# Kernel optimization log

Measured on AMD Instinct MI355X. Metric: run time of the kernel, lower is better.

## Reference

```python
import jax, jax.numpy as jnp
import numpy as np

B, S, D = 2, 2048, 2048
H = 16
HD = D // H
SCALE = 1.0 / (HD ** 0.5)


def setup_inputs() -> dict:
    key = jax.random.key(0)
    ks = jax.random.split(key, 9)
    std = 0.02
    return {
        "x": jax.random.normal(ks[0], (B, S, D), dtype=jnp.float32),
        "q_w": jax.random.normal(ks[1], (D, D), dtype=jnp.float32) * std,
        "q_b": jax.random.normal(ks[2], (D,), dtype=jnp.float32) * std,
        "k_w": jax.random.normal(ks[3], (D, D), dtype=jnp.float32) * std,
        "k_b": jax.random.normal(ks[4], (D,), dtype=jnp.float32) * std,
        "v_w": jax.random.normal(ks[5], (D, D), dtype=jnp.float32) * std,
        "v_b": jax.random.normal(ks[6], (D,), dtype=jnp.float32) * std,
        "o_w": jax.random.normal(ks[7], (D, D), dtype=jnp.float32) * std,
        "o_b": jax.random.normal(ks[8], (D,), dtype=jnp.float32) * std,
    }


def reference(x, q_w, q_b, k_w, k_b, v_w, v_b, o_w, o_b):
    # torch Linear: y = x @ W.T + b  (weights stored [out, in])
    b, s, _ = x.shape
    dtype = x.dtype
    q = (x @ q_w.T + q_b).reshape(b, s, H, HD).transpose(0, 2, 1, 3)  # [B,H,S,HD]
    k = (x @ k_w.T + k_b).reshape(b, s, H, HD).transpose(0, 2, 1, 3)
    v = (x @ v_w.T + v_b).reshape(b, s, H, HD).transpose(0, 2, 1, 3)
    scores = jnp.einsum("bhqd,bhkd->bhqk", q, k) * SCALE  # [B,H,S,S]
    # causal mask: positions k > q get -inf (via triu(diagonal=1))
    causal = jnp.triu(jnp.ones((s, s), dtype=bool), k=1)
    scores = jnp.where(causal[None, None], -jnp.inf, scores)
    attn = jax.nn.softmax(scores.astype(jnp.float32), axis=-1).astype(dtype)
    out = jnp.einsum("bhqk,bhkd->bhqd", attn, v)  # [B,H,S,HD]
    out = out.transpose(0, 2, 1, 3).reshape(b, s, H * HD)
    return out @ o_w.T + o_b
```

## Files before the change

kernel.cpp:

```cpp
#include <hip/hip_runtime.h>
#include <hip/hip_bf16.h>

#define S_LEN 2048
#define DMODEL 2048
#define NH 16
#define HDIM 128
#define SCALE_F 0.08838834764831845f

typedef __attribute__((ext_vector_type(8))) short bf16x8;
typedef __attribute__((ext_vector_type(4))) float f32x4;

__device__ __forceinline__ unsigned short f2bf(float f) {
  unsigned int u = __float_as_uint(f);
  u += 0x7FFFu + ((u >> 16) & 1u);
  return (unsigned short)(u >> 16);
}

__device__ __forceinline__ void gload16(const void* g, void* l) {
  __builtin_amdgcn_global_load_lds(
      (const __attribute__((address_space(1))) unsigned int*)g,
      (__attribute__((address_space(3))) unsigned int*)l, 16, 0, 0);
}

__global__ __launch_bounds__(256) void cvt_f32_bf16(
    const float* __restrict__ in, unsigned short* __restrict__ out, int n4) {
  int i = blockIdx.x * blockDim.x + threadIdx.x;
  if (i < n4) {
    const float4 v = *(const float4*)(in + i * 4);
    ushort4 o;
    o.x = f2bf(v.x); o.y = f2bf(v.y); o.z = f2bf(v.z); o.w = f2bf(v.w);
    *(ushort4*)(out + i * 4) = o;
  }
}

__global__ __launch_bounds__(256, 2) void gemm_qkv(
    const unsigned short* __restrict__ A,
    const unsigned short* __restrict__ W,
    const float* __restrict__ qbias, const float* __restrict__ kbias,
    const float* __restrict__ vbias,
    unsigned short* __restrict__ qo, unsigned short* __restrict__ ko,
    unsigned short* __restrict__ vto) {
  __shared__ unsigned short As[128 * 32];
  __shared__ unsigned short Bs[128 * 32];
  const int t = threadIdx.x;
  const int lane = t & 63;
  const int w = t >> 6;
  const int m0 = blockIdx.x * 128;
  const int n0 = blockIdx.y * 128;
  const int wr = w >> 1, wc = w & 1;

  f32x4 acc[4][4];
#pragma unroll
  for (int i = 0; i < 4; i++)
#pragma unroll
    for (int j = 0; j < 4; j++)
#pragma unroll
      for (int e = 0; e < 4; e++) acc[i][j][e] = 0.f;

  const int r0 = t >> 2;
  const int kc0 = (t & 3) * 8;
  const unsigned short* Arow0 = A + (m0 + r0) * DMODEL + kc0;
  const unsigned short* Arow1 = A + (m0 + 64 + r0) * DMODEL + kc0;
  const unsigned short* Wrow0 = W + (n0 + r0) * DMODEL + kc0;
  const unsigned short* Wrow1 = W + (n0 + 64 + r0) * DMODEL + kc0;
  char* AsB = (char*)As;
  char* BsB = (char*)Bs;

  const int frow = lane & 15;
  const int fcol = (lane >> 4) * 8;

  for (int k0 = 0; k0 < DMODEL; k0 += 32) {
    __syncthreads();
    gload16(Arow0 + k0, AsB + w * 1024);
    gload16(Arow1 + k0, AsB + 4096 + w * 1024);
    gload16(Wrow0 + k0, BsB + w * 1024);
    gload16(Wrow1 + k0, BsB + 4096 + w * 1024);
    __syncthreads();
    bf16x8 af[4], bfr[4];
#pragma unroll
    for (int i = 0; i < 4; i++)
      af[i] = *(const bf16x8*)&As[(wr * 64 + i * 16 + frow) * 32 + fcol];
#pragma unroll
    for (int j = 0; j < 4; j++)
      bfr[j] = *(const bf16x8*)&Bs[(wc * 64 + j * 16 + frow) * 32 + fcol];
#pragma unroll
    for (int i = 0; i < 4; i++)
#pragma unroll
      for (int j = 0; j < 4; j++)
        acc[i][j] = __builtin_amdgcn_mfma_f32_16x16x32_bf16(af[i], bfr[j],
                                                            acc[i][j], 0, 0, 0);
  }

  const int b_ = m0 >> 11;
  const int proj = n0 >> 11;
  const int nn_base = (n0 & 2047) + wc * 64;
  const float* bias = (proj == 0) ? qbias : ((proj == 1) ? kbias : vbias);
#pragma unroll
  for (int j = 0; j < 4; j++) {
    const int nn = nn_base + j * 16 + (lane & 15);
    const int h = nn >> 7, hd = nn & 127;
    const float bv = bias[nn];
#pragma unroll
    for (int i = 0; i < 4; i++) {
      const int mrow = m0 + wr * 64 + i * 16 + (lane >> 4) * 4;
      const int s = mrow & 2047;
      if (proj == 2) {
        unsigned short* dst = vto + ((b_ * NH + h) * HDIM + hd) * S_LEN + s;
        ushort4 pk;
        pk.x = f2bf(acc[i][j][0] + bv);
        pk.y = f2bf(acc[i][j][1] + bv);
        pk.z = f2bf(acc[i][j][2] + bv);
        pk.w = f2bf(acc[i][j][3] + bv);
        *(ushort4*)dst = pk;
      } else {
        unsigned short* dst =
            ((proj == 0) ? qo : ko) + ((b_ * NH + h) * S_LEN + s) * HDIM + hd;
#pragma unroll
        for (int r = 0; r < 4; r++) dst[r * HDIM] = f2bf(acc[i][j][r] + bv);
      }
    }
  }
}

__global__ __launch_bounds__(256, 2) void attn_fwd(
    const unsigned short* __restrict__ Q,
    const unsigned short* __restrict__ K,
    const unsigned short* __restrict__ VT,
    unsigned short* __restrict__ ctx) {
  __shared__ unsigned short Ks[2][64 * 128];
  __shared__ unsigned short Vs[2][128 * 64];
  __shared__ unsigned short Ps[4][16 * 64];
  const int t = threadIdx.x, lane = t & 63, w = t >> 6;
  const int bh = blockIdx.y;
  const unsigned short* Qb = Q + bh * (S_LEN * HDIM);
  const unsigned short* Kb = K + bh * (S_LEN * HDIM);
  const unsigned short* Vb = VT + bh * (HDIM * S_LEN);
  const int b_ = bh >> 4, h = bh & 15;

  const int krow_s = t >> 2;
  const int kchunk = t & 3;

  auto stageKV = [&](int buf, int kv0) {
#pragma unroll
    for (int u = 0; u < 4; ++u) {
      const int c = t + u * 256;
      const int row = c >> 4, cc = c & 15;
      gload16(Kb + (kv0 + row) * HDIM + ((cc ^ (row & 7)) * 8),
              (char*)Ks[buf] + u * 4096 + w * 1024);
    }
#pragma unroll
    for (int u = 0; u < 4; ++u) {
      const int c = t + u * 256;
      const int row = c >> 3, cc = c & 7;
      gload16(Vb + row * S_LEN + kv0 + ((cc ^ (row & 7)) * 8),
              (char*)Vs[buf] + u * 4096 + w * 1024);
    }
  };

#pragma unroll 1
  for (int pi = 0; pi < 2; ++pi) {
    const int qtile = pi ? (31 - blockIdx.x) : blockIdx.x;
    const int q0 = qtile * 64 + w * 16;

    bf16x8 qf[4];
    {
      const unsigned short* qrow =
          Qb + (q0 + (lane & 15)) * HDIM + (lane >> 4) * 8;
#pragma unroll
      for (int dk = 0; dk < 4; dk++) qf[dk] = *(const bf16x8*)(qrow + dk * 32);
    }

    float mrow[4], lrow[4];
    f32x4 oacc[8];
#pragma unroll
    for (int r = 0; r < 4; r++) { mrow[r] = -__builtin_inff(); lrow[r] = 0.f; }
#pragma unroll
    for (int d = 0; d < 8; d++)
#pragma unroll
      for (int e = 0; e < 4; e++) oacc[d][e] = 0.f;

    const int nt = qtile + 1;
    stageKV(0, 0);
    __syncthreads();
    int cur = 0;

#pragma unroll 1
    for (int kt = 0; kt < nt; ++kt) {
      if (kt + 1 < nt) stageKV(cur ^ 1, (kt + 1) * 64);

      const unsigned short* Kc = Ks[cur];
      const unsigned short* Vc = Vs[cur];
      const int kv0 = kt * 64;

      f32x4 sacc[4];
#pragma unroll
      for (int ck = 0; ck < 4; ck++)
#pragma unroll
        for (int e = 0; e < 4; e++) sacc[ck][e] = 0.f;
      __builtin_amdgcn_s_setprio(1);
#pragma unroll
      for (int ck = 0; ck < 4; ++ck) {
        const int krow = ck * 16 + (lane & 15);
#pragma unroll
        for (int dk = 0; dk < 4; ++dk) {
          const int chunk = dk * 4 + (lane >> 4);
          const bf16x8 kf = *(const bf16x8*)((const char*)Kc + krow * 256 +
                                             ((chunk ^ (krow & 7)) << 4));
          sacc[ck] = __builtin_amdgcn_mfma_f32_16x16x32_bf16(qf[dk], kf,
                                                             sacc[ck], 0, 0, 0);
        }
      }
      __builtin_amdgcn_s_setprio(0);
#pragma unroll
      for (int ck = 0; ck < 4; ck++)
#pragma unroll
        for (int r = 0; r < 4; r++) sacc[ck][r] *= SCALE_F;
      if (kt == qtile) {
#pragma unroll
        for (int ck = 0; ck < 4; ck++) {
          const int col = kv0 + ck * 16 + (lane & 15);
#pragma unroll
          for (int r = 0; r < 4; r++) {
            const int rowq = q0 + (lane >> 4) * 4 + r;
            if (col > rowq) sacc[ck][r] = -__builtin_inff();
          }
        }
      }
      float tmax[4];
#pragma unroll
      for (int r = 0; r < 4; r++)
        tmax[r] = fmaxf(fmaxf(sacc[0][r], sacc[1][r]),
                        fmaxf(sacc[2][r], sacc[3][r]));
#pragma unroll
      for (int off = 1; off < 16; off <<= 1)
#pragma unroll
        for (int r = 0; r < 4; r++)
          tmax[r] = fmaxf(tmax[r], __shfl_xor(tmax[r], off, 64));
      bool need = false;
#pragma unroll
      for (int r = 0; r < 4; r++) need |= (tmax[r] > mrow[r] + 8.f);
      if (__any(need)) {
#pragma unroll
        for (int r = 0; r < 4; r++) {
          const float mn = fmaxf(mrow[r], tmax[r]);
          const float corr = __expf(mrow[r] - mn);
          mrow[r] = mn;
          lrow[r] *= corr;
#pragma unroll
          for (int d = 0; d < 8; d++) oacc[d][r] *= corr;
        }
      }
      float rsum[4] = {0.f, 0.f, 0.f, 0.f};
#pragma unroll
      for (int ck = 0; ck < 4; ck++)
#pragma unroll
        for (int r = 0; r < 4; r++) {
          const float p = __expf(sacc[ck][r] - mrow[r]);
          rsum[r] += p;
          const int prow = (lane >> 4) * 4 + r;
          const int pcol = ck * 16 + (lane & 15);
          *(unsigned short*)((char*)Ps[w] +
                             ((prow * 128 + pcol * 2) ^ ((prow & 7) << 4))) =
              f2bf(p);
        }
#pragma unroll
      for (int off = 1; off < 16; off <<= 1)
#pragma unroll
        for (int r = 0; r < 4; r++) rsum[r] += __shfl_xor(rsum[r], off, 64);
#pragma unroll
      for (int r = 0; r < 4; r++) lrow[r] += rsum[r];

      bf16x8 pf[2];
      {
        const int prow = lane & 15;
#pragma unroll
        for (int kk = 0; kk < 2; kk++) {
          const int chunk = kk * 4 + (lane >> 4);
          pf[kk] = *(const bf16x8*)((const char*)Ps[w] + prow * 128 +
                                    ((chunk ^ (prow & 7)) << 4));
        }
      }
      __builtin_amdgcn_s_setprio(1);
#pragma unroll
      for (int d = 0; d < 8; ++d) {
        const int vrow = d * 16 + (lane & 15);
#pragma unroll
        for (int kk = 0; kk < 2; ++kk) {
          const int chunk = kk * 4 + (lane >> 4);
          const bf16x8 vf = *(const bf16x8*)((const char*)Vc + vrow * 128 +
                                             ((chunk ^ (vrow & 7)) << 4));
          oacc[d] = __builtin_amdgcn_mfma_f32_16x16x32_bf16(pf[kk], vf, oacc[d],
                                                            0, 0, 0);
        }
      }
      __builtin_amdgcn_s_setprio(0);

      __syncthreads();
      cur ^= 1;
    }

#pragma unroll
    for (int r = 0; r < 4; r++) {
      const float inv = 1.f / lrow[r];
      const int srow = q0 + (lane >> 4) * 4 + r;
      unsigned short* dst =
          ctx + (b_ * S_LEN + srow) * DMODEL + h * HDIM + (lane & 15);
#pragma unroll
      for (int d = 0; d < 8; d++) dst[d * 16] = f2bf(oacc[d][r] * inv);
    }
  }
}

__global__ __launch_bounds__(256, 2) void gemm_out(
    const unsigned short* __restrict__ A,
    const unsigned short* __restrict__ W,
    const float* __restrict__ bias, float* __restrict__ out) {
  __shared__ unsigned short As[128 * 32];
  __shared__ unsigned short Bs[128 * 32];
  const int t = threadIdx.x;
  const int lane = t & 63;
  const int w = t >> 6;
  const int m0 = blockIdx.x * 128;
  const int n0 = blockIdx.y * 128;
  const int wr = w >> 1, wc = w & 1;

  f32x4 acc[4][4];
#pragma unroll
  for (int i = 0; i < 4; i++)
#pragma unroll
    for (int j = 0; j < 4; j++)
#pragma unroll
      for (int e = 0; e < 4; e++) acc[i][j][e] = 0.f;

  const int r0 = t >> 2;
  const int kc0 = (t & 3) * 8;
  const unsigned short* Arow0 = A + (m0 + r0) * DMODEL + kc0;
  const unsigned short* Arow1 = A + (m0 + 64 + r0) * DMODEL + kc0;
  const unsigned short* Wrow0 = W + (n0 + r0) * DMODEL + kc0;
  const unsigned short* Wrow1 = W + (n0 + 64 + r0) * DMODEL + kc0;
  char* AsB = (char*)As;
  char* BsB = (char*)Bs;
  const int frow = lane & 15;
  const int fcol = (lane >> 4) * 8;

  for (int k0 = 0; k0 < DMODEL; k0 += 32) {
    __syncthreads();
    gload16(Arow0 + k0, AsB + w * 1024);
    gload16(Arow1 + k0, AsB + 4096 + w * 1024);
    gload16(Wrow0 + k0, BsB + w * 1024);
    gload16(Wrow1 + k0, BsB + 4096 + w * 1024);
    __syncthreads();
    bf16x8 af[4], bfr[4];
#pragma unroll
    for (int i = 0; i < 4; i++)
      af[i] = *(const bf16x8*)&As[(wr * 64 + i * 16 + frow) * 32 + fcol];
#pragma unroll
    for (int j = 0; j < 4; j++)
      bfr[j] = *(const bf16x8*)&Bs[(wc * 64 + j * 16 + frow) * 32 + fcol];
#pragma unroll
    for (int i = 0; i < 4; i++)
#pragma unroll
      for (int j = 0; j < 4; j++)
        acc[i][j] = __builtin_amdgcn_mfma_f32_16x16x32_bf16(af[i], bfr[j],
                                                            acc[i][j], 0, 0, 0);
  }

#pragma unroll
  for (int j = 0; j < 4; j++) {
    const int n = n0 + wc * 64 + j * 16 + (lane & 15);
    const float bv = bias[n];
#pragma unroll
    for (int i = 0; i < 4; i++) {
      const int mrow = m0 + wr * 64 + i * 16 + (lane >> 4) * 4;
      float* dst = out + mrow * DMODEL + n;
#pragma unroll
      for (int r = 0; r < 4; r++) dst[r * DMODEL] = acc[i][j][r] + bv;
    }
  }
}

extern "C" void kernel_launch(void* const* d_in, const int* in_sizes, int n_in,
                              void* d_out, int out_size, void* d_ws,
                              size_t ws_size, hipStream_t stream) {
  const float* x  = (const float*)d_in[0];
  const float* qw = (const float*)d_in[1];
  const float* qb = (const float*)d_in[2];
  const float* kw = (const float*)d_in[3];
  const float* kb = (const float*)d_in[4];
  const float* vw = (const float*)d_in[5];
  const float* vb = (const float*)d_in[6];
  const float* ow = (const float*)d_in[7];
  const float* ob = (const float*)d_in[8];
  float* out = (float*)d_out;

  unsigned short* xb   = (unsigned short*)d_ws;
  unsigned short* wqkv = xb + (size_t)8388608;
  unsigned short* wo   = wqkv + (size_t)12582912;
  unsigned short* qt_  = wo + (size_t)4194304;
  unsigned short* kt_  = qt_ + (size_t)8388608;
  unsigned short* vt_  = kt_ + (size_t)8388608;
  unsigned short* ctx  = vt_ + (size_t)8388608;

  cvt_f32_bf16<<<8192, 256, 0, stream>>>(x, xb, 2097152);
  cvt_f32_bf16<<<4096, 256, 0, stream>>>(qw, wqkv, 1048576);
  cvt_f32_bf16<<<4096, 256, 0, stream>>>(kw, wqkv + 4194304, 1048576);
  cvt_f32_bf16<<<4096, 256, 0, stream>>>(vw, wqkv + 8388608, 1048576);
  cvt_f32_bf16<<<4096, 256, 0, stream>>>(ow, wo, 1048576);

  gemm_qkv<<<dim3(32, 48), 256, 0, stream>>>(xb, wqkv, qb, kb, vb, qt_, kt_, vt_);
  attn_fwd<<<dim3(16, 32), 256, 0, stream>>>(qt_, kt_, vt_, ctx);
  gemm_out<<<dim3(32, 16), 256, 0, stream>>>(ctx, wo, ob, out);
}
```

Baseline: 293.2 us.

## Rewrite projection GEMMs with 128x256 tiles, multi-stage LDS pipeline, and fused conversion

Both projection GEMMs now share a new core that uses 512-thread blocks with 128x256 output tiles. It keeps a 96KB multi-buffered LDS ring filled by asynchronous global-to-LDS loads overlapped with MFMA, uses a swizzled LDS layout to avoid bank conflicts, and remaps block IDs to improve L2 reuse. The five float-to-bf16 conversion launches are merged into one kernel to cut launch overhead. The gains come from fewer barriers per unit of work and from load/compute overlap. In exchange, occupancy drops to one block per CU and the wait-count pipelining is fragile.

Result: slower. 299.5 us (+2.2%).

```diff
diff --git a/kernel.cpp b/kernel.cpp
--- a/kernel.cpp
+++ b/kernel.cpp
@@ -22,102 +22,186 @@
       (__attribute__((address_space(3))) unsigned int*)l, 16, 0, 0);
 }
 
-__global__ __launch_bounds__(256) void cvt_f32_bf16(
-    const float* __restrict__ in, unsigned short* __restrict__ out, int n4) {
+__global__ __launch_bounds__(256) void cvt_all(
+    const float* __restrict__ x, const float* __restrict__ qw,
+    const float* __restrict__ kw, const float* __restrict__ vw,
+    const float* __restrict__ ow, unsigned short* __restrict__ xb,
+    unsigned short* __restrict__ wqkv, unsigned short* __restrict__ wo) {
   int i = blockIdx.x * blockDim.x + threadIdx.x;
-  if (i < n4) {
-    const float4 v = *(const float4*)(in + i * 4);
-    ushort4 o;
-    o.x = f2bf(v.x); o.y = f2bf(v.y); o.z = f2bf(v.z); o.w = f2bf(v.w);
-    *(ushort4*)(out + i * 4) = o;
+  const float* src;
+  unsigned short* dst;
+  int off;
+  if (i < 2097152) {
+    src = x; dst = xb; off = i;
+  } else {
+    const int j = i - 2097152;
+    const int wsel = j >> 20;
+    off = j & 1048575;
+    src = (wsel == 0) ? qw : (wsel == 1) ? kw : (wsel == 2) ? vw : ow;
+    dst = (wsel == 0) ? wqkv
+        : (wsel == 1) ? (wqkv + 4194304)
+        : (wsel == 2) ? (wqkv + 8388608)
+                      : wo;
   }
-}
-
-__global__ __launch_bounds__(256, 2) void gemm_qkv(
-    const unsigned short* __restrict__ A,
-    const unsigned short* __restrict__ W,
+  const float4 v = *(const float4*)(src + (size_t)off * 4);
+  ushort4 o;
+  o.x = f2bf(v.x); o.y = f2bf(v.y); o.z = f2bf(v.z); o.w = f2bf(v.w);
+  *(ushort4*)(dst + (size_t)off * 4) = o;
+}
+
+__device__ __forceinline__ void gemm_core_128x256(
+    const unsigned short* __restrict__ Ag, const unsigned short* __restrict__ Wg,
+    int m0, int n0, char* lds, int t, f32x4 (&acc)[4][4]) {
+  const int lane = t & 63, w = t >> 6;
+  const int wr = w >> 2, wc = w & 3;
+
+#pragma unroll
+  for (int mi = 0; mi < 4; ++mi)
+#pragma unroll
+    for (int nj = 0; nj < 4; ++nj)
+#pragma unroll
+      for (int e = 0; e < 4; ++e) acc[mi][nj][e] = 0.f;
+
+  const int fr = lane & 15;
+  const int sw16 = (((lane >> 4) ^ ((lane >> 1) & 3)) << 4);
+  const int aRowBase = (wr * 64 + fr) * 64;
+  const int bRowBase = (wc * 64 + fr) * 64;
+
+  const int cg8 = (((t & 3) ^ ((t >> 3) & 3)) * 8);
+  const unsigned short* sAbase = Ag + (m0 + (t >> 2)) * DMODEL + cg8;
+  const unsigned short* sBbase0 = Wg + (n0 + (t >> 2)) * DMODEL + cg8;
+  const unsigned short* sBbase1 = sBbase0 + 128 * DMODEL;
+  char* dstW = lds + w * 1024;
+
+#pragma unroll
+  for (int T = 0; T < 2; ++T)
+#pragma unroll
+    for (int h = 0; h < 2; ++h) {
+      const int koff = T * 64 + h * 32;
+      const int aoff = T * 16384 + h * 8192;
+      const int boff = 32768 + T * 32768 + h * 16384;
+      gload16(sAbase + koff, dstW + aoff);
+      gload16(sBbase0 + koff, dstW + boff);
+      gload16(sBbase1 + koff, dstW + boff + 8192);
+    }
+  asm volatile("s_waitcnt vmcnt(0)" ::: "memory");
+  __builtin_amdgcn_s_barrier();
+
+#pragma unroll 1
+  for (int it = 0; it < 16; ++it) {
+#pragma unroll
+    for (int ph = 0; ph < 4; ++ph) {
+      const int rA = (ph >> 1) * 16384 + (ph & 1) * 8192;
+      const int rB = 32768 + (ph >> 1) * 32768 + (ph & 1) * 16384;
+      bf16x8 a[4], b[4];
+#pragma unroll
+      for (int mi = 0; mi < 4; ++mi)
+        a[mi] = *(const bf16x8*)(lds + rA + aRowBase + mi * 1024 + sw16);
+#pragma unroll
+      for (int nj = 0; nj < 4; ++nj)
+        b[nj] = *(const bf16x8*)(lds + rB + bRowBase + nj * 1024 + sw16);
+
+      const int SB_[4] = {1, 0, 0, 1};
+      const int SH_[4] = {1, 0, 1, 0};
+      const int TO_[4] = {1, 2, 2, 3};
+      if (!(ph == 0 && it == 0)) {
+        const int Tc = (2 * it + TO_[ph]) & 31;
+        const int koff = Tc * 64 + SH_[ph] * 32;
+        const int aoff = SB_[ph] * 16384 + SH_[ph] * 8192;
+        const int boff = 32768 + SB_[ph] * 32768 + SH_[ph] * 16384;
+        gload16(sAbase + koff, dstW + aoff);
+        gload16(sBbase0 + koff, dstW + boff);
+        gload16(sBbase1 + koff, dstW + boff + 8192);
+      }
+      asm volatile("s_waitcnt vmcnt(3)" ::: "memory");
+      __builtin_amdgcn_s_barrier();
+      asm volatile("s_waitcnt lgkmcnt(0)" ::: "memory");
+      __builtin_amdgcn_sched_barrier(0);
+      __builtin_amdgcn_s_setprio(1);
+#pragma unroll
+      for (int mi = 0; mi < 4; ++mi)
+#pragma unroll
+        for (int nj = 0; nj < 4; ++nj)
+          acc[mi][nj] = __builtin_amdgcn_mfma_f32_16x16x32_bf16(
+              a[mi], b[nj], acc[mi][nj], 0, 0, 0);
+      __builtin_amdgcn_s_setprio(0);
+      __builtin_amdgcn_s_barrier();
+    }
+  }
+}
+
+__global__ __launch_bounds__(512, 1) void gemm_qkv(
+    const unsigned short* __restrict__ A, const unsigned short* __restrict__ W,
     const float* __restrict__ qbias, const float* __restrict__ kbias,
     const float* __restrict__ vbias,
     unsigned short* __restrict__ qo, unsigned short* __restrict__ ko,
     unsigned short* __restrict__ vto) {
-  __shared__ unsigned short As[128 * 32];
-  __shared__ unsigned short Bs[128 * 32];
+  extern __shared__ char lds[];
   const int t = threadIdx.x;
-  const int lane = t & 63;
-  const int w = t >> 6;
-  const int m0 = blockIdx.x * 128;
-  const int n0 = blockIdx.y * 128;
-  const int wr = w >> 1, wc = w & 1;
+  const int swz = ((int)blockIdx.x & 7) * 96 + ((int)blockIdx.x >> 3);
+  const int m0 = (swz & 31) * 128;
+  const int n0 = (swz >> 5) * 256;
 
   f32x4 acc[4][4];
-#pragma unroll
-  for (int i = 0; i < 4; i++)
-#pragma unroll
-    for (int j = 0; j < 4; j++)
-#pragma unroll
-      for (int e = 0; e < 4; e++) acc[i][j][e] = 0.f;
-
-  const int r0 = t >> 2;
-  const int kc0 = (t & 3) * 8;
-  const unsigned short* Arow0 = A + (m0 + r0) * DMODEL + kc0;
-  const unsigned short* Arow1 = A + (m0 + 64 + r0) * DMODEL + kc0;
-  const unsigned short* Wrow0 = W + (n0 + r0) * DMODEL + kc0;
-  const unsigned short* Wrow1 = W + (n0 + 64 + r0) * DMODEL + kc0;
-  char* AsB = (char*)As;
-  char* BsB = (char*)Bs;
-
-  const int frow = lane & 15;
-  const int fcol = (lane >> 4) * 8;
-
-  for (int k0 = 0; k0 < DMODEL; k0 += 32) {
-    __syncthreads();
-    gload16(Arow0 + k0, AsB + w * 1024);
-    gload16(Arow1 + k0, AsB + 4096 + w * 1024);
-    gload16(Wrow0 + k0, BsB + w * 1024);
-    gload16(Wrow1 + k0, BsB + 4096 + w * 1024);
-    __syncthreads();
-    bf16x8 af[4], bfr[4];
-#pragma unroll
-    for (int i = 0; i < 4; i++)
-      af[i] = *(const bf16x8*)&As[(wr * 64 + i * 16 + frow) * 32 + fcol];
-#pragma unroll
-    for (int j = 0; j < 4; j++)
-      bfr[j] = *(const bf16x8*)&Bs[(wc * 64 + j * 16 + frow) * 32 + fcol];
-#pragma unroll
-    for (int i = 0; i < 4; i++)
-#pragma unroll
-      for (int j = 0; j < 4; j++)
-        acc[i][j] = __builtin_amdgcn_mfma_f32_16x16x32_bf16(af[i], bfr[j],
-                                                            acc[i][j], 0, 0, 0);
-  }
-
+  gemm_core_128x256(A, W, m0, n0, lds, t, acc);
+
+  const int lane = t & 63, w = t >> 6;
+  const int wr = w >> 2, wc = w & 3;
   const int b_ = m0 >> 11;
   const int proj = n0 >> 11;
   const int nn_base = (n0 & 2047) + wc * 64;
   const float* bias = (proj == 0) ? qbias : ((proj == 1) ? kbias : vbias);
 #pragma unroll
-  for (int j = 0; j < 4; j++) {
-    const int nn = nn_base + j * 16 + (lane & 15);
+  for (int nj = 0; nj < 4; ++nj) {
+    const int nn = nn_base + nj * 16 + (lane & 15);
     const int h = nn >> 7, hd = nn & 127;
     const float bv = bias[nn];
 #pragma unroll
-    for (int i = 0; i < 4; i++) {
-      const int mrow = m0 + wr * 64 + i * 16 + (lane >> 4) * 4;
+    for (int mi = 0; mi < 4; ++mi) {
+      const int mrow = m0 + wr * 64 + mi * 16 + (lane >> 4) * 4;
       const int s = mrow & 2047;
       if (proj == 2) {
         unsigned short* dst = vto + ((b_ * NH + h) * HDIM + hd) * S_LEN + s;
         ushort4 pk;
-        pk.x = f2bf(acc[i][j][0] + bv);
-        pk.y = f2bf(acc[i][j][1] + bv);
-        pk.z = f2bf(acc[i][j][2] + bv);
-        pk.w = f2bf(acc[i][j][3] + bv);
+        pk.x = f2bf(acc[mi][nj][0] + bv);
+        pk.y = f2bf(acc[mi][nj][1] + bv);
+        pk.z = f2bf(acc[mi][nj][2] + bv);
+        pk.w = f2bf(acc[mi][nj][3] + bv);
         *(ushort4*)dst = pk;
       } else {
         unsigned short* dst =
             ((proj == 0) ? qo : ko) + ((b_ * NH + h) * S_LEN + s) * HDIM + hd;
 #pragma unroll
-        for (int r = 0; r < 4; r++) dst[r * HDIM] = f2bf(acc[i][j][r] + bv);
-      }
+        for (int r = 0; r < 4; r++) dst[r * HDIM] = f2bf(acc[mi][nj][r] + bv);
+      }
+    }
+  }
+}
+
+__global__ __launch_bounds__(512, 1) void gemm_out(
+    const unsigned short* __restrict__ A, const unsigned short* __restrict__ W,
+    const float* __restrict__ bias, float* __restrict__ out) {
+  extern __shared__ char lds[];
+  const int t = threadIdx.x;
+  const int swz = ((int)blockIdx.x & 7) * 32 + ((int)blockIdx.x >> 3);
+  const int m0 = (swz & 31) * 128;
+  const int n0 = (swz >> 5) * 256;
+
+  f32x4 acc[4][4];
+  gemm_core_128x256(A, W, m0, n0, lds, t, acc);
+
+  const int lane = t & 63, w = t >> 6;
+  const int wr = w >> 2, wc = w & 3;
+#pragma unroll
+  for (int nj = 0; nj < 4; ++nj) {
+    const int n = n0 + wc * 64 + nj * 16 + (lane & 15);
+    const float bv = bias[n];
+#pragma unroll
+    for (int mi = 0; mi < 4; ++mi) {
+      const int mrow = m0 + wr * 64 + mi * 16 + (lane >> 4) * 4;
+      float* dst = out + (size_t)mrow * DMODEL + n;
+#pragma unroll
+      for (int r = 0; r < 4; r++) dst[r * DMODEL] = acc[mi][nj][r] + bv;
     }
   }
 }
@@ -137,9 +221,6 @@
   const unsigned short* Vb = VT + bh * (HDIM * S_LEN);
   const int b_ = bh >> 4, h = bh & 15;
 
-  const int krow_s = t >> 2;
-  const int kchunk = t & 3;
-
   auto stageKV = [&](int buf, int kv0) {
 #pragma unroll
     for (int u = 0; u < 4; ++u) {
@@ -307,74 +388,6 @@
           ctx + (b_ * S_LEN + srow) * DMODEL + h * HDIM + (lane & 15);
 #pragma unroll
       for (int d = 0; d < 8; d++) dst[d * 16] = f2bf(oacc[d][r] * inv);
-    }
-  }
-}
-
-__global__ __launch_bounds__(256, 2) void gemm_out(
-    const unsigned short* __restrict__ A,
-    const unsigned short* __restrict__ W,
-    const float* __restrict__ bias, float* __restrict__ out) {
-  __shared__ unsigned short As[128 * 32];
-  __shared__ unsigned short Bs[128 * 32];
-  const int t = threadIdx.x;
-  const int lane = t & 63;
-  const int w = t >> 6;
-  const int m0 = blockIdx.x * 128;
-  const int n0 = blockIdx.y * 128;
-  const int wr = w >> 1, wc = w & 1;
-
-  f32x4 acc[4][4];
-#pragma unroll
-  for (int i = 0; i < 4; i++)
-#pragma unroll
-    for (int j = 0; j < 4; j++)
-#pragma unroll
-      for (int e = 0; e < 4; e++) acc[i][j][e] = 0.f;
-
-  const int r0 = t >> 2;
-  const int kc0 = (t & 3) * 8;
-  const unsigned short* Arow0 = A + (m0 + r0) * DMODEL + kc0;
-  const unsigned short* Arow1 = A + (m0 + 64 + r0) * DMODEL + kc0;
-  const unsigned short* Wrow0 = W + (n0 + r0) * DMODEL + kc0;
-  const unsigned short* Wrow1 = W + (n0 + 64 + r0) * DMODEL + kc0;
-  char* AsB = (char*)As;
-  char* BsB = (char*)Bs;
-  const int frow = lane & 15;
-  const int fcol = (lane >> 4) * 8;
-
-  for (int k0 = 0; k0 < DMODEL; k0 += 32) {
-    __syncthreads();
-    gload16(Arow0 + k0, AsB + w * 1024);
-    gload16(Arow1 + k0, AsB + 4096 + w * 1024);
-    gload16(Wrow0 + k0, BsB + w * 1024);
-    gload16(Wrow1 + k0, BsB + 4096 + w * 1024);
-    __syncthreads();
-    bf16x8 af[4], bfr[4];
-#pragma unroll
-    for (int i = 0; i < 4; i++)
-      af[i] = *(const bf16x8*)&As[(wr * 64 + i * 16 + frow) * 32 + fcol];
-#pragma unroll
-    for (int j = 0; j < 4; j++)
-      bfr[j] = *(const bf16x8*)&Bs[(wc * 64 + j * 16 + frow) * 32 + fcol];
-#pragma unroll
-    for (int i = 0; i < 4; i++)
-#pragma unroll
-      for (int j = 0; j < 4; j++)
-        acc[i][j] = __builtin_amdgcn_mfma_f32_16x16x32_bf16(af[i], bfr[j],
-                                                            acc[i][j], 0, 0, 0);
-  }
-
-#pragma unroll
-  for (int j = 0; j < 4; j++) {
-    const int n = n0 + wc * 64 + j * 16 + (lane & 15);
-    const float bv = bias[n];
-#pragma unroll
-    for (int i = 0; i < 4; i++) {
-      const int mrow = m0 + wr * 64 + i * 16 + (lane >> 4) * 4;
-      float* dst = out + mrow * DMODEL + n;
-#pragma unroll
-      for (int r = 0; r < 4; r++) dst[r * DMODEL] = acc[i][j][r] + bv;
     }
   }
 }
@@ -401,13 +414,9 @@
   unsigned short* vt_  = kt_ + (size_t)8388608;
   unsigned short* ctx  = vt_ + (size_t)8388608;
 
-  cvt_f32_bf16<<<8192, 256, 0, stream>>>(x, xb, 2097152);
-  cvt_f32_bf16<<<4096, 256, 0, stream>>>(qw, wqkv, 1048576);
-  cvt_f32_bf16<<<4096, 256, 0, stream>>>(kw, wqkv + 4194304, 1048576);
-  cvt_f32_bf16<<<4096, 256, 0, stream>>>(vw, wqkv + 8388608, 1048576);
-  cvt_f32_bf16<<<4096, 256, 0, stream>>>(ow, wo, 1048576);
-
-  gemm_qkv<<<dim3(32, 48), 256, 0, stream>>>(xb, wqkv, qb, kb, vb, qt_, kt_, vt_);
+  cvt_all<<<24576, 256, 0, stream>>>(x, qw, kw, vw, ow, xb, wqkv, wo);
+
+  gemm_qkv<<<768, 512, 98304, stream>>>(xb, wqkv, qb, kb, vb, qt_, kt_, vt_);
   attn_fwd<<<dim3(16, 32), 256, 0, stream>>>(qt_, kt_, vt_, ctx);
-  gemm_out<<<dim3(32, 16), 256, 0, stream>>>(ctx, wo, ob, out);
-}
+  gemm_out<<<256, 512, 98304, stream>>>(ctx, wo, ob, out);
+}
```
